# Optimization experiments

Measured on AMD Instinct MI355X. Metric: run time of the kernel, lower is better.

## Reference

```python
import jax, jax.numpy as jnp
import numpy as np

N_NODES = 100000
N_EDGES = 1600000
D_FEAT = 48


def setup_inputs() -> dict:
    key = jax.random.key(0)
    k1, k2, k3, k4 = jax.random.split(key, 4)
    rows = jax.random.randint(k1, (N_EDGES,), 0, N_NODES, dtype=jnp.int32)
    cols = jax.random.randint(k2, (N_EDGES,), 0, N_NODES, dtype=jnp.int32)
    vals = jax.random.uniform(k3, (N_EDGES,), dtype=jnp.float32)
    embeds = jax.random.normal(k4, (N_NODES, D_FEAT), dtype=jnp.float32)
    return {"rows": rows, "cols": cols, "vals": vals, "embeds": embeds}


def reference(rows, cols, vals, embeds):
    # out = spmm(adj, embeds): out[r] = sum_{e: rows[e]==r} vals[e] * embeds[cols[e]]
    msgs = vals[:, None] * embeds[cols]  # [E, d] gather + scale
    out = jax.ops.segment_sum(msgs, rows, num_segments=embeds.shape[0])  # [N, d]
    return out
```

## Files before the change

### kernel.cpp

```cpp
#include <hip/hip_runtime.h>
#include <hip/hip_fp16.h>


#define N_NODES 100000
#define N_EDGES 1600000
#define D_FEAT  48

#define RPB 64
#define NBUCKETS ((N_NODES + RPB - 1) / RPB)
#define NWG 128
#define CHUNK (N_EDGES / NWG)
#define MROW (NBUCKETS + 1)
#define CONV_N4 ((N_NODES * D_FEAT) / 4)
#define CONV_BLK ((CONV_N4 + 511) / 512)
#define CAP 1536

__global__ __launch_bounds__(512) void build_convert(const int* __restrict__ rows,
                                                     const int* __restrict__ cols,
                                                     const float* __restrict__ vals,
                                                     unsigned int* __restrict__ mat,
                                                     int2* __restrict__ buf1,
                                                     const float4* __restrict__ esrc,
                                                     __half2* __restrict__ edst) {
    const int t = threadIdx.x;
    if (blockIdx.x < NWG) {
        __shared__ unsigned int hist[NBUCKETS];
        __shared__ unsigned int part[512];
        const int w = blockIdx.x;
        for (int i = t; i < NBUCKETS; i += 512) hist[i] = 0u;
        __syncthreads();
        const int lo = w * CHUNK, hi = lo + CHUNK;
        for (int e = lo + t; e < hi; e += 512)
            atomicAdd(&hist[((unsigned)rows[e]) >> 6], 1u);
        __syncthreads();
        unsigned int c[4], sum = 0;
#pragma unroll
        for (int k = 0; k < 4; ++k) {
            int idx = t * 4 + k;
            c[k] = (idx < NBUCKETS) ? hist[idx] : 0u;
            sum += c[k];
        }
        part[t] = sum;
        __syncthreads();
        for (int off = 1; off < 512; off <<= 1) {
            unsigned int u = (t >= off) ? part[t - off] : 0u;
            __syncthreads();
            part[t] += u;
            __syncthreads();
        }
        unsigned int pre = (t == 0) ? 0u : part[t - 1];
        unsigned int* mrow = mat + (size_t)w * MROW;
#pragma unroll
        for (int k = 0; k < 4; ++k) {
            int idx = t * 4 + k;
            if (idx < NBUCKETS) {
                mrow[idx] = pre;
                hist[idx] = pre;
                pre += c[k];
            }
        }
        if (t == 0) mrow[NBUCKETS] = CHUNK;
        __syncthreads();
        for (int e = lo + t; e < hi; e += 512) {
            unsigned r = (unsigned)rows[e];
            unsigned b = r >> 6;
            unsigned pos = (unsigned)lo + atomicAdd(&hist[b], 1u);
            buf1[pos] = make_int2((int)(((r & 63u) << 17) | (unsigned)cols[e]),
                                  __float_as_int(vals[e]));
        }
    } else {
        int i = (blockIdx.x - NWG) * 512 + t;
        if (i < CONV_N4) {
            float4 v = esrc[i];
            edst[2 * i]     = __floats2half2_rn(v.x, v.y);
            edst[2 * i + 1] = __floats2half2_rn(v.z, v.w);
        }
    }
}

__global__ __launch_bounds__(512) void finalize_spmm(const unsigned int* __restrict__ mat,
                                                     const int2* __restrict__ buf1,
                                                     const __half2* __restrict__ embeds_h2,
                                                     float* __restrict__ out) {
    __shared__ unsigned int sedge[CAP];
    __shared__ unsigned int rstart[RPB + 1];
    __shared__ unsigned int rc[RPB];
    __shared__ unsigned int sscan[RPB];
    const int b = blockIdx.x, t = threadIdx.x;
    const int run  = t >> 2;
    const int sub4 = t & 3;
    const unsigned int* mr = mat + (size_t)run * MROW + b;
    const unsigned int s  = mr[0];
    const unsigned int e2 = mr[1];
    const unsigned int base = (unsigned)run * CHUNK;
    const int g   = t >> 5;
    const int sub = t & 31;
    const bool act = sub < 24;
    const int row0 = b * RPB;

#define PROC(q)                                                       \
    {                                                                 \
        union { __half h; unsigned short u; } hv;                     \
        hv.u = (unsigned short)((q) >> 17);                           \
        float vv = __half2float(hv.h);                                \
        __half2 e2v = embeds_h2[((q) & 0x1FFFFu) * 24 + sub];         \
        ax = fmaf(vv, __low2float(e2v), ax);                          \
        ay = fmaf(vv, __high2float(e2v), ay);                         \
    }

    if (t < RPB) rc[t] = 0u;
    __syncthreads();
    for (unsigned int k = s + sub4; k < e2; k += 4)
        atomicAdd(&rc[(unsigned)buf1[base + k].x >> 17], 1u);
    __syncthreads();
    if (t < RPB) sscan[t] = rc[t];
    __syncthreads();
    for (int off = 1; off < RPB; off <<= 1) {
        unsigned int u = 0;
        if (t < RPB && t >= off) u = sscan[t - off];
        __syncthreads();
        if (t < RPB && t >= off) sscan[t] += u;
        __syncthreads();
    }
    if (t < RPB) {
        unsigned int pre = (t == 0) ? 0u : sscan[t - 1];
        rstart[t] = pre;
        rc[t] = pre;
    }
    if (t == 0) rstart[RPB] = sscan[RPB - 1];
    __syncthreads();
    const unsigned int cnt = rstart[RPB];

    if (cnt <= CAP) {
        for (unsigned int k = s + sub4; k < e2; k += 4) {
            int2 cv = buf1[base + k];
            unsigned int pos = atomicAdd(&rc[(unsigned)cv.x >> 17], 1u);
            union { __half h; unsigned short u; } hv;
            hv.h = __float2half_rn(__int_as_float(cv.y));
            sedge[pos] = ((unsigned int)hv.u << 17) | ((unsigned)cv.x & 0x1FFFFu);
        }
        __syncthreads();

        for (int rr = g * 4; rr < g * 4 + 4; ++rr) {
            int row = row0 + rr;
            if (row >= N_NODES) break;
            unsigned int j = rstart[rr], end = rstart[rr + 1];
            float ax = 0.f, ay = 0.f;
            for (; j + 8 <= end; j += 8) {
                unsigned int q0 = sedge[j + 0];
                unsigned int q1 = sedge[j + 1];
                unsigned int q2 = sedge[j + 2];
                unsigned int q3 = sedge[j + 3];
                unsigned int q4 = sedge[j + 4];
                unsigned int q5 = sedge[j + 5];
                unsigned int q6 = sedge[j + 6];
                unsigned int q7 = sedge[j + 7];
                if (act) {
                    PROC(q0) PROC(q1) PROC(q2) PROC(q3)
                    PROC(q4) PROC(q5) PROC(q6) PROC(q7)
                }
            }
            for (; j < end; ++j) {
                unsigned int q = sedge[j];
                if (act) PROC(q)
            }
            if (act)
                *(float2*)(out + (size_t)row * D_FEAT + sub * 2) = make_float2(ax, ay);
        }
    } else {
        for (int rr = g * 4; rr < g * 4 + 4; ++rr) {
            int row = row0 + rr;
            if (row >= N_NODES) break;
            float ax = 0.f, ay = 0.f;
            for (int i = 0; i < NWG; ++i) {
                const unsigned int* mri = mat + (size_t)i * MROW + b;
                unsigned int si = mri[0], ei = mri[1];
                for (unsigned int k = si; k < ei; ++k) {
                    int2 cv = buf1[(unsigned)i * CHUNK + k];
                    if (((unsigned)cv.x >> 17) == (unsigned)rr && act) {
                        union { __half h; unsigned short u; } hv;
                        hv.h = __float2half_rn(__int_as_float(cv.y));
                        unsigned int q = ((unsigned int)hv.u << 17) | ((unsigned)cv.x & 0x1FFFFu);
                        PROC(q)
                    }
                }
            }
            if (act)
                *(float2*)(out + (size_t)row * D_FEAT + sub * 2) = make_float2(ax, ay);
        }
    }
#undef PROC
}

__global__ __launch_bounds__(256) void zero_out_kernel(float4* __restrict__ out, int n4) {
    int i = blockIdx.x * 256 + threadIdx.x;
    if (i < n4) out[i] = make_float4(0.f, 0.f, 0.f, 0.f);
}
__global__ __launch_bounds__(256) void spmm_atomic_kernel(const int* __restrict__ rows,
                                                          const int* __restrict__ cols,
                                                          const float* __restrict__ vals,
                                                          const float* __restrict__ embeds,
                                                          float* __restrict__ out) {
    long long tid = (long long)blockIdx.x * 256 + threadIdx.x;
    const long long total = (long long)N_EDGES * 12;
    if (tid >= total) return;
    int e = (int)(tid / 12), q = (int)(tid % 12);
    int r = rows[e], c = cols[e];
    float v = vals[e];
    const float4 emb = *(const float4*)(embeds + (long long)c * D_FEAT + q * 4);
    float* o = out + (long long)r * D_FEAT + q * 4;
    atomicAdd(o + 0, v * emb.x);
    atomicAdd(o + 1, v * emb.y);
    atomicAdd(o + 2, v * emb.z);
    atomicAdd(o + 3, v * emb.w);
}

extern "C" void kernel_launch(void* const* d_in, const int* in_sizes, int n_in,
                              void* d_out, int out_size, void* d_ws, size_t ws_size,
                              hipStream_t stream) {
    const int*   rows   = (const int*)d_in[0];
    const int*   cols   = (const int*)d_in[1];
    const float* vals   = (const float*)d_in[2];
    const float* embeds = (const float*)d_in[3];
    float*       out    = (float*)d_out;

    unsigned int* mat = (unsigned int*)d_ws;
    size_t mat_bytes  = ((size_t)NWG * MROW * 4 + 15) & ~(size_t)15;
    int2* buf1 = (int2*)((char*)d_ws + mat_bytes);
    __half2* embeds_h2 = (__half2*)((char*)buf1 + (size_t)N_EDGES * 8);
    size_t need = mat_bytes + (size_t)N_EDGES * 8 + (size_t)N_NODES * D_FEAT * 2;

    if (ws_size < need) {
        int n4 = out_size / 4;
        zero_out_kernel<<<(n4 + 255) / 256, 256, 0, stream>>>((float4*)out, n4);
        long long total = (long long)N_EDGES * 12;
        spmm_atomic_kernel<<<(int)((total + 255) / 256), 256, 0, stream>>>(rows, cols, vals, embeds, out);
        return;
    }

    build_convert<<<NWG + CONV_BLK, 512, 0, stream>>>(rows, cols, vals, mat, buf1,
                                                      (const float4*)embeds, embeds_h2);
    finalize_spmm<<<NBUCKETS, 512, 0, stream>>>(mat, buf1, embeds_h2, out);
}
```

Baseline: 83.02 us.

## Transpose bucket offset matrix, double build workgroups, and halve finalize block size

The per-workgroup bucket offset table is stored transposed (bucket-major), so each finalize block reads its start/end offsets for all runs as one contiguous, coalesced load instead of strided reads. The number of build workgroups doubles to 256, so each finalize thread owns exactly one run and walks it sequentially; before, four threads shared each run. The finalize block shrinks to 256 threads, with each 32-lane group accumulating 8 rows instead of 4. The trade-off is less parallelism per block in the accumulation phase, serial per-thread loops over run segments, and a larger offset table.

```diff
diff --git a/kernel.cpp b/kernel.cpp
--- a/kernel.cpp
+++ b/kernel.cpp
@@ -8,7 +8,7 @@
 
 #define RPB 64
 #define NBUCKETS ((N_NODES + RPB - 1) / RPB)
-#define NWG 128
+#define NWG 256
 #define CHUNK (N_EDGES / NWG)
 #define MROW (NBUCKETS + 1)
 #define CONV_N4 ((N_NODES * D_FEAT) / 4)
@@ -18,7 +18,7 @@
 __global__ __launch_bounds__(512) void build_convert(const int* __restrict__ rows,
                                                      const int* __restrict__ cols,
                                                      const float* __restrict__ vals,
-                                                     unsigned int* __restrict__ mat,
+                                                     unsigned int* __restrict__ matT,
                                                      int2* __restrict__ buf1,
                                                      const float4* __restrict__ esrc,
                                                      __half2* __restrict__ edst) {
@@ -49,17 +49,16 @@
             __syncthreads();
         }
         unsigned int pre = (t == 0) ? 0u : part[t - 1];
-        unsigned int* mrow = mat + (size_t)w * MROW;
 #pragma unroll
         for (int k = 0; k < 4; ++k) {
             int idx = t * 4 + k;
             if (idx < NBUCKETS) {
-                mrow[idx] = pre;
+                matT[(size_t)idx * NWG + w] = pre;
                 hist[idx] = pre;
                 pre += c[k];
             }
         }
-        if (t == 0) mrow[NBUCKETS] = CHUNK;
+        if (t == 0) matT[(size_t)NBUCKETS * NWG + w] = CHUNK;
         __syncthreads();
         for (int e = lo + t; e < hi; e += 512) {
             unsigned r = (unsigned)rows[e];
@@ -78,7 +77,7 @@
     }
 }
 
-__global__ __launch_bounds__(512) void finalize_spmm(const unsigned int* __restrict__ mat,
+__global__ __launch_bounds__(256) void finalize_spmm(const unsigned int* __restrict__ matT,
                                                      const int2* __restrict__ buf1,
                                                      const __half2* __restrict__ embeds_h2,
                                                      float* __restrict__ out) {
@@ -87,12 +86,9 @@
     __shared__ unsigned int rc[RPB];
     __shared__ unsigned int sscan[RPB];
     const int b = blockIdx.x, t = threadIdx.x;
-    const int run  = t >> 2;
-    const int sub4 = t & 3;
-    const unsigned int* mr = mat + (size_t)run * MROW + b;
-    const unsigned int s  = mr[0];
-    const unsigned int e2 = mr[1];
-    const unsigned int base = (unsigned)run * CHUNK;
+    const unsigned int s  = matT[(size_t)b * NWG + t];
+    const unsigned int e2 = matT[(size_t)(b + 1) * NWG + t];
+    const unsigned int base = (unsigned)t * CHUNK;
     const int g   = t >> 5;
     const int sub = t & 31;
     const bool act = sub < 24;
@@ -110,7 +106,7 @@
 
     if (t < RPB) rc[t] = 0u;
     __syncthreads();
-    for (unsigned int k = s + sub4; k < e2; k += 4)
+    for (unsigned int k = s; k < e2; ++k)
         atomicAdd(&rc[(unsigned)buf1[base + k].x >> 17], 1u);
     __syncthreads();
     if (t < RPB) sscan[t] = rc[t];
@@ -132,7 +128,7 @@
     const unsigned int cnt = rstart[RPB];
 
     if (cnt <= CAP) {
-        for (unsigned int k = s + sub4; k < e2; k += 4) {
+        for (unsigned int k = s; k < e2; ++k) {
             int2 cv = buf1[base + k];
             unsigned int pos = atomicAdd(&rc[(unsigned)cv.x >> 17], 1u);
             union { __half h; unsigned short u; } hv;
@@ -141,7 +137,7 @@
         }
         __syncthreads();
 
-        for (int rr = g * 4; rr < g * 4 + 4; ++rr) {
+        for (int rr = g * 8; rr < g * 8 + 8; ++rr) {
             int row = row0 + rr;
             if (row >= N_NODES) break;
             unsigned int j = rstart[rr], end = rstart[rr + 1];
@@ -168,13 +164,13 @@
                 *(float2*)(out + (size_t)row * D_FEAT + sub * 2) = make_float2(ax, ay);
         }
     } else {
-        for (int rr = g * 4; rr < g * 4 + 4; ++rr) {
+        for (int rr = g * 8; rr < g * 8 + 8; ++rr) {
             int row = row0 + rr;
             if (row >= N_NODES) break;
             float ax = 0.f, ay = 0.f;
             for (int i = 0; i < NWG; ++i) {
-                const unsigned int* mri = mat + (size_t)i * MROW + b;
-                unsigned int si = mri[0], ei = mri[1];
+                unsigned int si = matT[(size_t)b * NWG + i];
+                unsigned int ei = matT[(size_t)(b + 1) * NWG + i];
                 for (unsigned int k = si; k < ei; ++k) {
                     int2 cv = buf1[(unsigned)i * CHUNK + k];
                     if (((unsigned)cv.x >> 17) == (unsigned)rr && act) {
@@ -224,8 +220,8 @@
     const float* embeds = (const float*)d_in[3];
     float*       out    = (float*)d_out;
 
-    unsigned int* mat = (unsigned int*)d_ws;
-    size_t mat_bytes  = ((size_t)NWG * MROW * 4 + 15) & ~(size_t)15;
+    unsigned int* matT = (unsigned int*)d_ws;
+    size_t mat_bytes  = ((size_t)MROW * NWG * 4 + 15) & ~(size_t)15;
     int2* buf1 = (int2*)((char*)d_ws + mat_bytes);
     __half2* embeds_h2 = (__half2*)((char*)buf1 + (size_t)N_EDGES * 8);
     size_t need = mat_bytes + (size_t)N_EDGES * 8 + (size_t)N_NODES * D_FEAT * 2;
@@ -238,7 +234,7 @@
         return;
     }
 
-    build_convert<<<NWG + CONV_BLK, 512, 0, stream>>>(rows, cols, vals, mat, buf1,
+    build_convert<<<NWG + CONV_BLK, 512, 0, stream>>>(rows, cols, vals, matT, buf1,
                                                       (const float4*)embeds, embeds_h2);
-    finalize_spmm<<<NBUCKETS, 512, 0, stream>>>(mat, buf1, embeds_h2, out);
-}
+    finalize_spmm<<<NBUCKETS, 256, 0, stream>>>(matT, buf1, embeds_h2, out);
+}
```

New measurement: 102.8 us. 23.8% more time.
